# Optimization experiments

Hardware: AMD Instinct MI355X
Metric: run time of the kernel (lower is better)

Reference implementation:

```python
import jax, jax.numpy as jnp
import numpy as np

D_MODEL = 1024
N_HEAD = 16
D_HEAD = D_MODEL // N_HEAD
D_FF = 4096
B, S = 2, 2048
EPS = 1e-5


def setup_inputs() -> dict:
    key = jax.random.key(0)
    ks = jax.random.split(key, 16)
    sc = 1.0 / np.sqrt(D_MODEL)
    x = jax.random.normal(ks[0], (B, S, D_MODEL), dtype=jnp.float32)
    # causal mask: 1 where attention is disallowed (upper triangle)
    mask = jnp.triu(jnp.ones((S, S), dtype=jnp.int32), k=1)[None, None]
    p = {
        'x': x,
        'mask': mask,
        'wq': jax.random.normal(ks[1], (D_MODEL, D_MODEL), jnp.float32) * sc,
        'bq': jnp.zeros((D_MODEL,), jnp.float32),
        'wk': jax.random.normal(ks[2], (D_MODEL, D_MODEL), jnp.float32) * sc,
        'bk': jnp.zeros((D_MODEL,), jnp.float32),
        'wv': jax.random.normal(ks[3], (D_MODEL, D_MODEL), jnp.float32) * sc,
        'bv': jnp.zeros((D_MODEL,), jnp.float32),
        'wo': jax.random.normal(ks[4], (D_MODEL, D_MODEL), jnp.float32) * sc,
        'bo': jnp.zeros((D_MODEL,), jnp.float32),
        'w1': jax.random.normal(ks[5], (D_MODEL, D_FF), jnp.float32) * sc,
        'b1': jnp.zeros((D_FF,), jnp.float32),
        'w2': jax.random.normal(ks[6], (D_FF, D_MODEL), jnp.float32) * (1.0 / np.sqrt(D_FF)),
        'b2': jnp.zeros((D_MODEL,), jnp.float32),
        'g1': jnp.ones((D_MODEL,), jnp.float32),
        'beta1': jnp.zeros((D_MODEL,), jnp.float32),
        'g2': jnp.ones((D_MODEL,), jnp.float32),
        'beta2': jnp.zeros((D_MODEL,), jnp.float32),
    }
    return p


def _layer_norm(x, g, b):
    mu = jnp.mean(x, axis=-1, keepdims=True)
    var = jnp.mean(jnp.square(x - mu), axis=-1, keepdims=True)
    return (x - mu) * jax.lax.rsqrt(var + EPS) * g + b


def reference(x, mask, wq, bq, wk, bk, wv, bv, wo, bo, w1, b1, w2, b2, g1, beta1, g2, beta2):
    b, s, _ = x.shape
    # QKV projections -> [B, H, S, Dh]
    q = (x @ wq + bq).reshape(b, s, N_HEAD, D_HEAD).transpose(0, 2, 1, 3)
    k = (x @ wk + bk).reshape(b, s, N_HEAD, D_HEAD).transpose(0, 2, 1, 3)
    v = (x @ wv + bv).reshape(b, s, N_HEAD, D_HEAD).transpose(0, 2, 1, 3)
    scores = jnp.einsum('bhqd,bhkd->bhqk', q, k) / np.sqrt(D_HEAD)  # [B,H,S,S]
    scores = jnp.where(mask == 1, -jnp.inf, scores)
    attn = jax.nn.softmax(scores, axis=-1)
    out = jnp.einsum('bhqk,bhkd->bhqd', attn, v)
    out = out.transpose(0, 2, 1, 3).reshape(b, s, D_MODEL)
    attn_out = out @ wo + bo
    x1 = _layer_norm(x + attn_out, g1, beta1)
    ffn = jax.nn.relu(x1 @ w1 + b1) @ w2 + b2
    return _layer_norm(x1 + ffn, g2, beta2)
```

## Files before the change

### kernel.cpp

```cpp
#include <hip/hip_runtime.h>
#include <hip/hip_bf16.h>
#include <cstdint>

#define D_MODEL 1024
#define D_FF    4096
#define NHEAD   16
#define DHEAD   64
#define BATCH   2
#define SEQ     2048
#define BT      (BATCH*SEQ)
#define QKVLD   (3*D_MODEL)
#define LN_EPS  1e-5f

typedef __bf16 bf16_t;
typedef bf16_t bf16x8 __attribute__((ext_vector_type(8)));
typedef float  f32x4  __attribute__((ext_vector_type(4)));

__device__ __forceinline__ unsigned short f2b(float f){
  bf16_t h = (bf16_t)f;
  return __builtin_bit_cast(unsigned short, h);
}

__device__ __forceinline__ void gload16(const void* g, void* l){
  __builtin_amdgcn_global_load_lds(
      (const __attribute__((address_space(1))) unsigned int*)g,
      (__attribute__((address_space(3))) unsigned int*)l, 16, 0, 0);
}

__global__ __launch_bounds__(256) void cvt_f32_bf16(
    const float* __restrict__ in, unsigned short* __restrict__ out, int n){
  int i = (blockIdx.x*256 + threadIdx.x)*4;
  if (i < n){
    float4 v = *(const float4*)(in + i);
    ushort4 u; u.x=f2b(v.x); u.y=f2b(v.y); u.z=f2b(v.z); u.w=f2b(v.w);
    *(ushort4*)(out + i) = u;
  }
}

__global__ __launch_bounds__(256) void concat_bias(
    const float* __restrict__ bq, const float* __restrict__ bk,
    const float* __restrict__ bv, float* __restrict__ o){
  int i = blockIdx.x*256 + threadIdx.x;
  if (i < D_MODEL){ o[i]=bq[i]; o[D_MODEL+i]=bk[i]; o[2*D_MODEL+i]=bv[i]; }
}

__global__ __launch_bounds__(256) void transpose_cvt(
    const float* __restrict__ in, unsigned short* __restrict__ out, int R, int C){
  __shared__ float t[32][33];
  int c0 = blockIdx.x*32, r0 = blockIdx.y*32;
  int tx = threadIdx.x, ty = threadIdx.y;
  #pragma unroll
  for (int i=0;i<4;++i){ int r = ty + i*8; t[r][tx] = in[(size_t)(r0+r)*C + c0+tx]; }
  __syncthreads();
  #pragma unroll
  for (int i=0;i<4;++i){ int r = ty + i*8; out[(size_t)(c0+r)*R + r0+tx] = f2b(t[tx][r]); }
}

__global__ __launch_bounds__(256) void transpose_v(
    const unsigned short* __restrict__ QKV, unsigned short* __restrict__ Vt){
  __shared__ unsigned short t[32][33];
  int s0 = blockIdx.x*32, d0 = blockIdx.y*32, bh = blockIdx.z;
  int b = bh>>4, h = bh&15;
  int tx = threadIdx.x, ty = threadIdx.y;
  #pragma unroll
  for (int i=0;i<4;++i){ int r = ty + i*8;
    t[r][tx] = QKV[(size_t)(b*SEQ + s0+r)*QKVLD + 2*D_MODEL + h*DHEAD + d0+tx]; }
  __syncthreads();
  #pragma unroll
  for (int i=0;i<4;++i){ int r = ty + i*8;
    Vt[((size_t)bh*DHEAD + d0+r)*SEQ + s0+tx] = t[tx][r]; }
}

template<int EPI>
__global__ __launch_bounds__(512,4) void gemm128(
    const unsigned short* __restrict__ A, const unsigned short* __restrict__ Bt,
    const float* __restrict__ bias, const float* __restrict__ resid,
    float* __restrict__ outF, unsigned short* __restrict__ outB,
    int M, int N, int K){
  __shared__ __attribute__((aligned(16))) unsigned short As[2][128*64];
  __shared__ __attribute__((aligned(16))) unsigned short Bs[2][128*64];
  int tid = threadIdx.x;
  int lane = tid & 63, wave = tid >> 6;
  int lr = lane & 15, lg = lane >> 4;
  int row0 = blockIdx.x*128, col0 = blockIdx.y*128;
  int wr = (wave>>2)*64, wc = (wave&3)*32;
  int x7 = lr & 7;

  int sr = tid >> 3;
  int sl = (tid & 7) ^ (sr & 7);
  auto STAGE = [&](int k0, int buf){
    #pragma unroll
    for (int it=0; it<2; ++it){
      int c = it*512 + tid;
      int r = it*64 + sr;
      gload16(A  + (size_t)(row0+r)*K + k0 + sl*8, &As[buf][c<<3]);
      gload16(Bt + (size_t)(col0+r)*K + k0 + sl*8, &Bs[buf][c<<3]);
    }
  };

  f32x4 acc[4][2] = {};
  int nk = K >> 6;
  int t0 = 0, t1 = nk;
  if (EPI==3){ int half = nk >> 1; t0 = blockIdx.z*half; t1 = t0 + half; }
  STAGE(t0<<6, 0);
  asm volatile("s_waitcnt vmcnt(0)" ::: "memory");
  __builtin_amdgcn_s_barrier();
  int cur = 0;
  for (int t=t0; t<t1; ++t){
    if (t+1 < t1) STAGE((t+1)<<6, cur^1);
    #pragma unroll
    for (int kk=0; kk<2; ++kk){
      int sk = ((kk*4 + lg) ^ x7) << 3;
      bf16x8 af[4], bfr[2];
      #pragma unroll
      for (int mi=0;mi<4;++mi) af[mi]  = *(const bf16x8*)&As[cur][(wr+mi*16+lr)*64 + sk];
      #pragma unroll
      for (int ni=0;ni<2;++ni) bfr[ni] = *(const bf16x8*)&Bs[cur][(wc+ni*16+lr)*64 + sk];
      #pragma unroll
      for (int mi=0;mi<4;++mi)
        #pragma unroll
        for (int ni=0;ni<2;++ni)
          acc[mi][ni] = __builtin_amdgcn_mfma_f32_16x16x32_bf16(af[mi], bfr[ni], acc[mi][ni], 0,0,0);
    }
    asm volatile("s_waitcnt vmcnt(0)" ::: "memory");
    __builtin_amdgcn_s_barrier();
    cur ^= 1;
  }
  float* outP = (EPI==3) ? (outF + (size_t)blockIdx.z*((size_t)M*N)) : outF;
  #pragma unroll
  for (int mi=0;mi<4;++mi){
    int row = row0 + wr + mi*16 + (lg<<2);
    #pragma unroll
    for (int ni=0;ni<2;++ni){
      int col = col0 + wc + ni*16 + lr;
      float bs = (EPI==3) ? 0.f : bias[col];
      #pragma unroll
      for (int j=0;j<4;++j){
        size_t idx = (size_t)(row+j)*N + col;
        float v = acc[mi][ni][j] + bs;
        if (EPI==3){ outP[idx] = v; }
        else if (EPI==2){ v = fmaxf(v, 0.f); outB[idx] = f2b(v); }
        else { outB[idx] = f2b(v); }
      }
    }
  }
}

__global__ __launch_bounds__(256,2) void attn_k(
    const unsigned short* __restrict__ QKV,
    const unsigned short* __restrict__ Vt, unsigned short* __restrict__ O){
  __shared__ __attribute__((aligned(16))) unsigned short Ks[2][128*64];
  __shared__ __attribute__((aligned(16))) unsigned short Vs[2][64*128];
  __shared__ __attribute__((aligned(16))) unsigned short Ps[4][16*128];
  int tid = threadIdx.x, lane = tid&63, wave = tid>>6;
  int lr = lane&15, lg = lane>>4;
  int bid = blockIdx.x;
  int L = (bid & 7)*64 + (bid >> 3);
  int qx = L & 15;
  int bh = L >> 4;
  int b = bh>>4, h = bh&15;
  const int NT = SEQ/64;
  const float SC2 = 0.18033688011112042f;

  #pragma unroll 1
  for (int half=0; half<2; ++half){
    int qt = half ? qx : (NT-1 - qx);
    int q0w = qt*64 + wave*16;

    const unsigned short* Qrow = QKV + (size_t)(b*SEQ + q0w + lr)*QKVLD + h*DHEAD;
    bf16x8 qf[2];
    qf[0] = *(const bf16x8*)(Qrow + lg*8);
    qf[1] = *(const bf16x8*)(Qrow + 32 + lg*8);

    f32x4 oacc[4] = {};
    float m2 = -1e30f, lsum = 0.f;

    auto STAGE = [&](int t, int buf){
      int kv0 = t*128;
      #pragma unroll
      for (int it=0; it<4; ++it){
        int c = it*256 + tid;
        int rk = c>>3, slk = (c&7) ^ (rk&7);
        gload16(QKV + (size_t)(b*SEQ + kv0 + rk)*QKVLD + D_MODEL + h*DHEAD + slk*8, &Ks[buf][c<<3]);
        int rv = c>>4, slv = (c&15) ^ (rv&15);
        gload16(Vt + ((size_t)bh*DHEAD + rv)*SEQ + kv0 + slv*8, &Vs[buf][c<<3]);
      }
    };

    int nkv = (qt + 2) >> 1;
    STAGE(0, 0);
    asm volatile("s_waitcnt vmcnt(0)" ::: "memory");
    __builtin_amdgcn_s_barrier();
    int cur = 0;
    for (int t=0; t<nkv; ++t){
      if (t+1 < nkv) STAGE(t+1, cur^1);

      int kv0 = t*128;
      f32x4 sacc[8] = {};
      #pragma unroll
      for (int kk=0;kk<2;++kk){
        #pragma unroll
        for (int ni=0;ni<8;++ni){
          int krow = ni*16 + lr;
          bf16x8 kf = *(const bf16x8*)&Ks[cur][krow*64 + (((kk*4+lg) ^ (krow&7))<<3)];
          sacc[ni] = __builtin_amdgcn_mfma_f32_16x16x32_bf16(kf, qf[kk], sacc[ni], 0,0,0);
        }
      }
      if (t == nkv-1){
        int qpos = q0w + lr;
        #pragma unroll
        for (int ni=0;ni<8;++ni){
          f32x4 v = sacc[ni];
          #pragma unroll
          for (int j=0;j<4;++j){
            int kpos = kv0 + ni*16 + lg*4 + j;
            float sv = v[j]*SC2;
            v[j] = (kpos > qpos) ? -1e30f : sv;
          }
          sacc[ni] = v;
        }
      } else {
        #pragma unroll
        for (int ni=0;ni<8;++ni) sacc[ni] *= SC2;
      }
      f32x4 vm = sacc[0];
      #pragma unroll
      for (int ni=1;ni<8;++ni)
        #pragma unroll
        for (int j=0;j<4;++j) vm[j] = fmaxf(vm[j], sacc[ni][j]);
      float rm = fmaxf(fmaxf(vm[0],vm[1]), fmaxf(vm[2],vm[3]));
      rm = fmaxf(rm, __shfl_xor(rm, 16));
      rm = fmaxf(rm, __shfl_xor(rm, 32));
      float mnew = fmaxf(m2, rm);
      float corr = exp2f(m2 - mnew);
      m2 = mnew;
      f32x4 vs = {};
      #pragma unroll
      for (int ni=0;ni<8;++ni){
        f32x4 p;
        #pragma unroll
        for (int j=0;j<4;++j){ p[j] = exp2f(sacc[ni][j] - mnew); vs[j] += p[j]; }
        sacc[ni] = p;
      }
      float rs = (vs[0]+vs[1]) + (vs[2]+vs[3]);
      rs += __shfl_xor(rs, 16);
      rs += __shfl_xor(rs, 32);
      lsum = lsum*corr + rs;
      #pragma unroll
      for (int j=0;j<4;++j){
        float cj = __shfl(corr, lg*4 + j);
        #pragma unroll
        for (int nd=0; nd<4; ++nd) oacc[nd][j] *= cj;
      }
      #pragma unroll
      for (int ni=0;ni<8;++ni){
        ushort4 u; u.x=f2b(sacc[ni][0]); u.y=f2b(sacc[ni][1]);
                   u.z=f2b(sacc[ni][2]); u.w=f2b(sacc[ni][3]);
        int ts = ni*2 + (lg>>1);
        int a = lr*128 + (((ts ^ lr))<<3) + ((lg&1)<<2);
        *(uint2*)&Ps[wave][a] = __builtin_bit_cast(uint2, u);
      }
      #pragma unroll
      for (int kk=0;kk<4;++kk){
        bf16x8 pa = *(const bf16x8*)&Ps[wave][lr*128 + (((kk*4+lg) ^ lr)<<3)];
        #pragma unroll
        for (int nd=0; nd<4; ++nd){
          int dr = nd*16 + lr;
          bf16x8 vf = *(const bf16x8*)&Vs[cur][dr*128 + (((kk*4+lg) ^ (dr&15))<<3)];
          oacc[nd] = __builtin_amdgcn_mfma_f32_16x16x32_bf16(pa, vf, oacc[nd], 0,0,0);
        }
      }
      asm volatile("s_waitcnt vmcnt(0)" ::: "memory");
      __builtin_amdgcn_s_barrier();
      cur ^= 1;
    }
    #pragma unroll
    for (int j=0;j<4;++j){
      float lj = __shfl(lsum, lg*4 + j);
      float inv = 1.f / lj;
      int token = b*SEQ + q0w + lg*4 + j;
      #pragma unroll
      for (int nd=0; nd<4; ++nd)
        O[(size_t)token*D_MODEL + h*DHEAD + nd*16 + lr] = f2b(oacc[nd][j]*inv);
    }
  }
}

template<int MODE>
__global__ __launch_bounds__(256) void ln_sum_k(
    const float* __restrict__ P,
    const float* __restrict__ bias,
    const float* __restrict__ resid,
    const float* __restrict__ g, const float* __restrict__ bta,
    float* __restrict__ outF, unsigned short* __restrict__ outB){
  int row = blockIdx.x, tid = threadIdx.x;
  const size_t MN = (size_t)BT*D_MODEL;
  float4 p0 = ((const float4*)(P + (size_t)row*D_MODEL))[tid];
  float4 p1 = ((const float4*)(P + MN + (size_t)row*D_MODEL))[tid];
  float4 rr = ((const float4*)(resid + (size_t)row*D_MODEL))[tid];
  float4 bb = ((const float4*)bias)[tid];
  float4 v;
  v.x = p0.x+p1.x+bb.x+rr.x; v.y = p0.y+p1.y+bb.y+rr.y;
  v.z = p0.z+p1.z+bb.z+rr.z; v.w = p0.w+p1.w+bb.w+rr.w;
  float s = v.x+v.y+v.z+v.w;
  float q = v.x*v.x+v.y*v.y+v.z*v.z+v.w*v.w;
  #pragma unroll
  for (int d=32; d; d>>=1){ s += __shfl_xor(s, d); q += __shfl_xor(q, d); }
  __shared__ float rs[4], rq[4];
  int wave = tid>>6;
  if ((tid&63)==0){ rs[wave]=s; rq[wave]=q; }
  __syncthreads();
  s = rs[0]+rs[1]+rs[2]+rs[3];
  q = rq[0]+rq[1]+rq[2]+rq[3];
  float mu  = s * (1.f/D_MODEL);
  float var = q * (1.f/D_MODEL) - mu*mu;
  float rstd = rsqrtf(var + LN_EPS);
  float4 gg = ((const float4*)g)[tid];
  float4 be = ((const float4*)bta)[tid];
  float o0 = (v.x-mu)*rstd*gg.x + be.x;
  float o1 = (v.y-mu)*rstd*gg.y + be.y;
  float o2 = (v.z-mu)*rstd*gg.z + be.z;
  float o3 = (v.w-mu)*rstd*gg.w + be.w;
  float4 o; o.x=o0; o.y=o1; o.z=o2; o.w=o3;
  ((float4*)(outF + (size_t)row*D_MODEL))[tid] = o;
  if (MODE==0){
    ushort4 u; u.x=f2b(o0); u.y=f2b(o1); u.z=f2b(o2); u.w=f2b(o3);
    ((ushort4*)(outB + (size_t)row*D_MODEL))[tid] = u;
  }
}

extern "C" void kernel_launch(void* const* d_in, const int* in_sizes, int n_in,
                              void* d_out, int out_size, void* d_ws, size_t ws_size,
                              hipStream_t stream){
  const float* x  = (const float*)d_in[0];
  const float* wq = (const float*)d_in[2];  const float* bq = (const float*)d_in[3];
  const float* wk = (const float*)d_in[4];  const float* bk = (const float*)d_in[5];
  const float* wv = (const float*)d_in[6];  const float* bv = (const float*)d_in[7];
  const float* wo = (const float*)d_in[8];  const float* bo = (const float*)d_in[9];
  const float* w1 = (const float*)d_in[10]; const float* b1 = (const float*)d_in[11];
  const float* w2 = (const float*)d_in[12]; const float* b2 = (const float*)d_in[13];
  const float* g1 = (const float*)d_in[14]; const float* be1= (const float*)d_in[15];
  const float* g2 = (const float*)d_in[16]; const float* be2= (const float*)d_in[17];

  char* w = (char*)d_ws;
  size_t off = 0;
  auto nxt = [&](size_t bytes)->void*{
    void* p = w + off; off = (off + bytes + 255) & ~(size_t)255; return p;
  };
  unsigned short* xb    = (unsigned short*)nxt((size_t)BT*D_MODEL*2);
  unsigned short* wqkvT = (unsigned short*)nxt((size_t)QKVLD*D_MODEL*2);
  unsigned short* woT   = (unsigned short*)nxt((size_t)D_MODEL*D_MODEL*2);
  unsigned short* w1T   = (unsigned short*)nxt((size_t)D_MODEL*D_FF*2);
  unsigned short* w2T   = (unsigned short*)nxt((size_t)D_MODEL*D_FF*2);
  float*          bqkv  = (float*)nxt((size_t)QKVLD*4);
  unsigned short* QKV   = (unsigned short*)nxt((size_t)BT*QKVLD*2);
  unsigned short* VtG   = (unsigned short*)nxt((size_t)BT*D_MODEL*2);
  unsigned short* attnb = (unsigned short*)nxt((size_t)BT*D_MODEL*2);
  float*          x1f   = (float*)nxt((size_t)BT*D_MODEL*4);
  unsigned short* ffn1  = (unsigned short*)nxt((size_t)BT*D_FF*2);
  float*          Psum  = (float*)QKV;
  unsigned short* x1b   = attnb;

  dim3 tb(32,8);
  cvt_f32_bf16<<<(BT*D_MODEL)/1024, 256, 0, stream>>>(x, xb, BT*D_MODEL);
  concat_bias<<<4, 256, 0, stream>>>(bq, bk, bv, bqkv);
  transpose_cvt<<<dim3(D_MODEL/32, D_MODEL/32), tb, 0, stream>>>(wq, wqkvT,                    D_MODEL, D_MODEL);
  transpose_cvt<<<dim3(D_MODEL/32, D_MODEL/32), tb, 0, stream>>>(wk, wqkvT + D_MODEL*D_MODEL,  D_MODEL, D_MODEL);
  transpose_cvt<<<dim3(D_MODEL/32, D_MODEL/32), tb, 0, stream>>>(wv, wqkvT + 2*D_MODEL*D_MODEL,D_MODEL, D_MODEL);
  transpose_cvt<<<dim3(D_MODEL/32, D_MODEL/32), tb, 0, stream>>>(wo, woT, D_MODEL, D_MODEL);
  transpose_cvt<<<dim3(D_FF/32,    D_MODEL/32), tb, 0, stream>>>(w1, w1T, D_MODEL, D_FF);
  transpose_cvt<<<dim3(D_MODEL/32, D_FF/32),    tb, 0, stream>>>(w2, w2T, D_FF, D_MODEL);

  gemm128<0><<<dim3(BT/128, QKVLD/128), 512, 0, stream>>>(xb, wqkvT, bqkv, nullptr, nullptr, QKV, BT, QKVLD, D_MODEL);

  transpose_v<<<dim3(SEQ/32, DHEAD/32, BATCH*NHEAD), tb, 0, stream>>>(QKV, VtG);
  attn_k<<<512, 256, 0, stream>>>(QKV, VtG, attnb);

  gemm128<3><<<dim3(BT/128, D_MODEL/128, 2), 512, 0, stream>>>(attnb, woT, nullptr, nullptr, Psum, nullptr, BT, D_MODEL, D_MODEL);
  ln_sum_k<0><<<BT, 256, 0, stream>>>(Psum, bo, x, g1, be1, x1f, x1b);

  gemm128<2><<<dim3(BT/128, D_FF/128), 512, 0, stream>>>(x1b, w1T, b1, nullptr, nullptr, ffn1, BT, D_FF, D_MODEL);

  gemm128<3><<<dim3(BT/128, D_MODEL/128, 2), 512, 0, stream>>>(ffn1, w2T, nullptr, nullptr, Psum, nullptr, BT, D_MODEL, D_FF);
  ln_sum_k<1><<<BT, 256, 0, stream>>>(Psum, b2, x1f, g2, be2, (float*)d_out, nullptr);
}
```

Baseline: 233.5 us.

## Give each attention wave two query groups and single-buffer V

The attention kernel now processes one 128-row query tile per block, with 32 rows per wave, instead of two 64-row tiles in a paired causal half loop. Each K/V fragment read from LDS feeds two MFMAs, which halves LDS traffic per unit of compute. V is single-buffered and its next tile is loaded after the PV stage, and the waits are relaxed to vmcnt(4) so K prefetch overlaps compute. The trade-offs are causal load imbalance across blocks (tile lengths range 1..16), higher register pressure, and V loads no longer overlapping the PV stage.

```diff
diff --git a/kernel.cpp b/kernel.cpp
--- a/kernel.cpp
+++ b/kernel.cpp
@@ -150,140 +150,163 @@
     const unsigned short* __restrict__ QKV,
     const unsigned short* __restrict__ Vt, unsigned short* __restrict__ O){
   __shared__ __attribute__((aligned(16))) unsigned short Ks[2][128*64];
-  __shared__ __attribute__((aligned(16))) unsigned short Vs[2][64*128];
-  __shared__ __attribute__((aligned(16))) unsigned short Ps[4][16*128];
+  __shared__ __attribute__((aligned(16))) unsigned short Vs[64*128];
+  __shared__ __attribute__((aligned(16))) unsigned short Ps[4][2][16*128];
   int tid = threadIdx.x, lane = tid&63, wave = tid>>6;
   int lr = lane&15, lg = lane>>4;
   int bid = blockIdx.x;
   int L = (bid & 7)*64 + (bid >> 3);
-  int qx = L & 15;
   int bh = L >> 4;
+  int qrank = L & 15;
+  int qt = 15 - qrank;
   int b = bh>>4, h = bh&15;
-  const int NT = SEQ/64;
+  int q0 = qt*128 + wave*32;
   const float SC2 = 0.18033688011112042f;
 
-  #pragma unroll 1
-  for (int half=0; half<2; ++half){
-    int qt = half ? qx : (NT-1 - qx);
-    int q0w = qt*64 + wave*16;
-
-    const unsigned short* Qrow = QKV + (size_t)(b*SEQ + q0w + lr)*QKVLD + h*DHEAD;
-    bf16x8 qf[2];
-    qf[0] = *(const bf16x8*)(Qrow + lg*8);
-    qf[1] = *(const bf16x8*)(Qrow + 32 + lg*8);
-
-    f32x4 oacc[4] = {};
-    float m2 = -1e30f, lsum = 0.f;
-
-    auto STAGE = [&](int t, int buf){
-      int kv0 = t*128;
-      #pragma unroll
-      for (int it=0; it<4; ++it){
-        int c = it*256 + tid;
-        int rk = c>>3, slk = (c&7) ^ (rk&7);
-        gload16(QKV + (size_t)(b*SEQ + kv0 + rk)*QKVLD + D_MODEL + h*DHEAD + slk*8, &Ks[buf][c<<3]);
-        int rv = c>>4, slv = (c&15) ^ (rv&15);
-        gload16(Vt + ((size_t)bh*DHEAD + rv)*SEQ + kv0 + slv*8, &Vs[buf][c<<3]);
-      }
-    };
-
-    int nkv = (qt + 2) >> 1;
-    STAGE(0, 0);
-    asm volatile("s_waitcnt vmcnt(0)" ::: "memory");
-    __builtin_amdgcn_s_barrier();
-    int cur = 0;
-    for (int t=0; t<nkv; ++t){
-      if (t+1 < nkv) STAGE(t+1, cur^1);
-
-      int kv0 = t*128;
-      f32x4 sacc[8] = {};
-      #pragma unroll
-      for (int kk=0;kk<2;++kk){
+  bf16x8 qf[2][2];
+  #pragma unroll
+  for (int g=0; g<2; ++g)
+    #pragma unroll
+    for (int kk=0; kk<2; ++kk)
+      qf[g][kk] = *(const bf16x8*)&QKV[(size_t)(b*SEQ + q0 + g*16 + lr)*QKVLD + h*DHEAD + kk*32 + lg*8];
+
+  f32x4 oacc[2][4] = {};
+  float m2[2] = {-1e30f, -1e30f}, lsum[2] = {0.f, 0.f};
+
+  auto STAGE_K = [&](int t, int buf){
+    int kv0 = t*128;
+    #pragma unroll
+    for (int it=0; it<4; ++it){
+      int c = it*256 + tid;
+      int rk = c>>3, slk = (c&7) ^ (rk&7);
+      gload16(QKV + (size_t)(b*SEQ + kv0 + rk)*QKVLD + D_MODEL + h*DHEAD + slk*8, &Ks[buf][c<<3]);
+    }
+  };
+  auto STAGE_V = [&](int t){
+    int kv0 = t*128;
+    #pragma unroll
+    for (int it=0; it<4; ++it){
+      int c = it*256 + tid;
+      int rv = c>>4, slv = (c&15) ^ (rv&15);
+      gload16(Vt + ((size_t)bh*DHEAD + rv)*SEQ + kv0 + slv*8, &Vs[c<<3]);
+    }
+  };
+
+  int nkv = qt + 1;
+  STAGE_K(0, 0);
+  STAGE_V(0);
+  asm volatile("s_waitcnt vmcnt(0)" ::: "memory");
+  __builtin_amdgcn_s_barrier();
+  int cur = 0;
+  for (int t=0; t<nkv; ++t){
+    bool pre = (t+1 < nkv);
+    if (pre) STAGE_K(t+1, cur^1);
+
+    int kv0 = t*128;
+    f32x4 sacc[2][8] = {};
+    #pragma unroll
+    for (int kk=0;kk<2;++kk){
+      #pragma unroll
+      for (int ni=0;ni<8;++ni){
+        int krow = ni*16 + lr;
+        bf16x8 kf = *(const bf16x8*)&Ks[cur][krow*64 + (((kk*4+lg) ^ (krow&7))<<3)];
+        sacc[0][ni] = __builtin_amdgcn_mfma_f32_16x16x32_bf16(kf, qf[0][kk], sacc[0][ni], 0,0,0);
+        sacc[1][ni] = __builtin_amdgcn_mfma_f32_16x16x32_bf16(kf, qf[1][kk], sacc[1][ni], 0,0,0);
+      }
+    }
+    if (t == nkv-1){
+      #pragma unroll
+      for (int g=0;g<2;++g){
+        int qpos = q0 + g*16 + lr;
         #pragma unroll
         for (int ni=0;ni<8;++ni){
-          int krow = ni*16 + lr;
-          bf16x8 kf = *(const bf16x8*)&Ks[cur][krow*64 + (((kk*4+lg) ^ (krow&7))<<3)];
-          sacc[ni] = __builtin_amdgcn_mfma_f32_16x16x32_bf16(kf, qf[kk], sacc[ni], 0,0,0);
-        }
-      }
-      if (t == nkv-1){
-        int qpos = q0w + lr;
-        #pragma unroll
-        for (int ni=0;ni<8;++ni){
-          f32x4 v = sacc[ni];
+          f32x4 v = sacc[g][ni];
           #pragma unroll
           for (int j=0;j<4;++j){
             int kpos = kv0 + ni*16 + lg*4 + j;
             float sv = v[j]*SC2;
             v[j] = (kpos > qpos) ? -1e30f : sv;
           }
-          sacc[ni] = v;
+          sacc[g][ni] = v;
         }
-      } else {
-        #pragma unroll
-        for (int ni=0;ni<8;++ni) sacc[ni] *= SC2;
-      }
-      f32x4 vm = sacc[0];
+      }
+    } else {
+      #pragma unroll
+      for (int g=0;g<2;++g)
+        #pragma unroll
+        for (int ni=0;ni<8;++ni) sacc[g][ni] *= SC2;
+    }
+    #pragma unroll
+    for (int g=0;g<2;++g){
+      f32x4 vm = sacc[g][0];
       #pragma unroll
       for (int ni=1;ni<8;++ni)
         #pragma unroll
-        for (int j=0;j<4;++j) vm[j] = fmaxf(vm[j], sacc[ni][j]);
+        for (int j=0;j<4;++j) vm[j] = fmaxf(vm[j], sacc[g][ni][j]);
       float rm = fmaxf(fmaxf(vm[0],vm[1]), fmaxf(vm[2],vm[3]));
       rm = fmaxf(rm, __shfl_xor(rm, 16));
       rm = fmaxf(rm, __shfl_xor(rm, 32));
-      float mnew = fmaxf(m2, rm);
-      float corr = exp2f(m2 - mnew);
-      m2 = mnew;
+      float mnew = fmaxf(m2[g], rm);
+      float corr = exp2f(m2[g] - mnew);
+      m2[g] = mnew;
       f32x4 vs = {};
       #pragma unroll
       for (int ni=0;ni<8;++ni){
         f32x4 p;
         #pragma unroll
-        for (int j=0;j<4;++j){ p[j] = exp2f(sacc[ni][j] - mnew); vs[j] += p[j]; }
-        sacc[ni] = p;
+        for (int j=0;j<4;++j){ p[j] = exp2f(sacc[g][ni][j] - mnew); vs[j] += p[j]; }
+        sacc[g][ni] = p;
       }
       float rs = (vs[0]+vs[1]) + (vs[2]+vs[3]);
       rs += __shfl_xor(rs, 16);
       rs += __shfl_xor(rs, 32);
-      lsum = lsum*corr + rs;
+      lsum[g] = lsum[g]*corr + rs;
       #pragma unroll
       for (int j=0;j<4;++j){
         float cj = __shfl(corr, lg*4 + j);
         #pragma unroll
-        for (int nd=0; nd<4; ++nd) oacc[nd][j] *= cj;
+        for (int nd=0; nd<4; ++nd) oacc[g][nd][j] *= cj;
       }
       #pragma unroll
       for (int ni=0;ni<8;++ni){
-        ushort4 u; u.x=f2b(sacc[ni][0]); u.y=f2b(sacc[ni][1]);
-                   u.z=f2b(sacc[ni][2]); u.w=f2b(sacc[ni][3]);
+        ushort4 u; u.x=f2b(sacc[g][ni][0]); u.y=f2b(sacc[g][ni][1]);
+                   u.z=f2b(sacc[g][ni][2]); u.w=f2b(sacc[g][ni][3]);
         int ts = ni*2 + (lg>>1);
-        int a = lr*128 + (((ts ^ lr))<<3) + ((lg&1)<<2);
-        *(uint2*)&Ps[wave][a] = __builtin_bit_cast(uint2, u);
-      }
-      #pragma unroll
-      for (int kk=0;kk<4;++kk){
-        bf16x8 pa = *(const bf16x8*)&Ps[wave][lr*128 + (((kk*4+lg) ^ lr)<<3)];
-        #pragma unroll
-        for (int nd=0; nd<4; ++nd){
-          int dr = nd*16 + lr;
-          bf16x8 vf = *(const bf16x8*)&Vs[cur][dr*128 + (((kk*4+lg) ^ (dr&15))<<3)];
-          oacc[nd] = __builtin_amdgcn_mfma_f32_16x16x32_bf16(pa, vf, oacc[nd], 0,0,0);
-        }
-      }
-      asm volatile("s_waitcnt vmcnt(0)" ::: "memory");
-      __builtin_amdgcn_s_barrier();
-      cur ^= 1;
-    }
+        int a = lr*128 + ((ts ^ lr)<<3) + ((lg&1)<<2);
+        *(uint2*)&Ps[wave][g][a] = __builtin_bit_cast(uint2, u);
+      }
+    }
+    if (pre){ asm volatile("s_waitcnt vmcnt(4)" ::: "memory"); }
+    else    { asm volatile("s_waitcnt vmcnt(0)" ::: "memory"); }
+    __builtin_amdgcn_s_barrier();
+    #pragma unroll
+    for (int kk=0;kk<4;++kk){
+      bf16x8 paA = *(const bf16x8*)&Ps[wave][0][lr*128 + (((kk*4+lg) ^ lr)<<3)];
+      bf16x8 paB = *(const bf16x8*)&Ps[wave][1][lr*128 + (((kk*4+lg) ^ lr)<<3)];
+      #pragma unroll
+      for (int nd=0; nd<4; ++nd){
+        int dr = nd*16 + lr;
+        bf16x8 vf = *(const bf16x8*)&Vs[dr*128 + (((kk*4+lg) ^ (dr&15))<<3)];
+        oacc[0][nd] = __builtin_amdgcn_mfma_f32_16x16x32_bf16(paA, vf, oacc[0][nd], 0,0,0);
+        oacc[1][nd] = __builtin_amdgcn_mfma_f32_16x16x32_bf16(paB, vf, oacc[1][nd], 0,0,0);
+      }
+    }
+    asm volatile("s_waitcnt vmcnt(0)" ::: "memory");
+    __builtin_amdgcn_s_barrier();
+    if (pre) STAGE_V(t+1);
+    cur ^= 1;
+  }
+  #pragma unroll
+  for (int g=0;g<2;++g)
     #pragma unroll
     for (int j=0;j<4;++j){
-      float lj = __shfl(lsum, lg*4 + j);
+      float lj = __shfl(lsum[g], lg*4 + j);
       float inv = 1.f / lj;
-      int token = b*SEQ + q0w + lg*4 + j;
+      int token = b*SEQ + q0 + g*16 + lg*4 + j;
       #pragma unroll
       for (int nd=0; nd<4; ++nd)
-        O[(size_t)token*D_MODEL + h*DHEAD + nd*16 + lr] = f2b(oacc[nd][j]*inv);
-    }
-  }
+        O[(size_t)token*D_MODEL + h*DHEAD + nd*16 + lr] = f2b(oacc[g][nd][j]*inv);
+    }
 }
 
 template<int MODE>
```

Measured after the change: 258.8 us. 10.8% more time.

## Add 256x256-tile GEMM with staged prefetch for QKV and FFN1 projections

Applied to the files above, without the earlier changes.

Adds a new GEMM kernel with 256x256 output tiles per 512-thread block. Each wave computes a 128x64 sub-tile in four quarter phases, and next-k-tile loads are interleaved between MFMA phases under s_setprio. The QKV and FFN-up GEMMs use it instead of the 128x128 kernel, which raises arithmetic intensity and cuts global/LDS traffic per FLOP. In exchange it uses 128KB of LDS per block and more accumulator registers, and launches fewer blocks (192 for QKV, 256 for FFN1), which may underfill the GPU's compute units.

```diff
diff --git a/kernel.cpp b/kernel.cpp
--- a/kernel.cpp
+++ b/kernel.cpp
@@ -141,6 +141,141 @@
         if (EPI==3){ outP[idx] = v; }
         else if (EPI==2){ v = fmaxf(v, 0.f); outB[idx] = f2b(v); }
         else { outB[idx] = f2b(v); }
+      }
+    }
+  }
+}
+
+template<int EPI>
+__global__ __launch_bounds__(512,2) void gemm256(
+    const unsigned short* __restrict__ A, const unsigned short* __restrict__ Bt,
+    const float* __restrict__ bias, unsigned short* __restrict__ outB,
+    int M, int N, int K){
+  __shared__ __attribute__((aligned(16))) unsigned short As[2][2][128*64];
+  __shared__ __attribute__((aligned(16))) unsigned short Bs[2][2][128*64];
+  int tid = threadIdx.x;
+  int lane = tid & 63, wave = tid >> 6;
+  int lr = lane & 15, lg = lane >> 4;
+  int wm = wave >> 2, wn = wave & 3;
+  int row0 = blockIdx.x*256, col0 = blockIdx.y*256;
+  int x7 = lr & 7;
+  int sr = tid >> 3;
+  int sl = (tid & 7) ^ (sr & 7);
+
+  auto STAGE_A = [&](int t, int buf, int h){
+    #pragma unroll
+    for (int i=0;i<2;++i){
+      int c = i*512 + tid;
+      int r = i*64 + sr;
+      gload16(A + (size_t)(row0 + h*128 + r)*K + t*64 + sl*8, &As[buf][h][c<<3]);
+    }
+  };
+  auto STAGE_B = [&](int t, int buf, int h){
+    #pragma unroll
+    for (int i=0;i<2;++i){
+      int c = i*512 + tid;
+      int r = i*64 + sr;
+      gload16(Bt + (size_t)(col0 + h*128 + r)*K + t*64 + sl*8, &Bs[buf][h][c<<3]);
+    }
+  };
+
+  f32x4 acc[8][4] = {};
+  int nk = K >> 6;
+  STAGE_B(0,0,0); STAGE_B(0,0,1); STAGE_A(0,0,0); STAGE_A(0,0,1);
+  asm volatile("s_waitcnt vmcnt(0)" ::: "memory");
+  __builtin_amdgcn_s_barrier();
+  int cur = 0;
+  int bq = (wn&1)*64;
+  for (int t=0; t<nk; ++t){
+    bool pre = (t+1 < nk);
+    const unsigned short* Ah = &As[cur][wm][0];
+    const unsigned short* Bh = &Bs[cur][wn>>1][0];
+    bf16x8 af[4][2], bfr[4][2];
+    #pragma unroll
+    for (int mi=0;mi<4;++mi)
+      #pragma unroll
+      for (int kk=0;kk<2;++kk)
+        af[mi][kk] = *(const bf16x8*)&Ah[(mi*16+lr)*64 + (((kk*4+lg)^x7)<<3)];
+    #pragma unroll
+    for (int ni=0;ni<2;++ni)
+      #pragma unroll
+      for (int kk=0;kk<2;++kk)
+        bfr[ni][kk] = *(const bf16x8*)&Bh[(bq+ni*16+lr)*64 + (((kk*4+lg)^x7)<<3)];
+    if (pre){ STAGE_B(t+1, cur^1, 0);
+              asm volatile("s_waitcnt vmcnt(2)" ::: "memory"); }
+    else    { asm volatile("s_waitcnt vmcnt(0)" ::: "memory"); }
+    __builtin_amdgcn_s_barrier();
+    __builtin_amdgcn_s_setprio(1);
+    #pragma unroll
+    for (int mi=0;mi<4;++mi)
+      #pragma unroll
+      for (int ni=0;ni<2;++ni)
+        #pragma unroll
+        for (int kk=0;kk<2;++kk)
+          acc[mi][ni] = __builtin_amdgcn_mfma_f32_16x16x32_bf16(af[mi][kk], bfr[ni][kk], acc[mi][ni], 0,0,0);
+    __builtin_amdgcn_s_setprio(0);
+    __builtin_amdgcn_s_barrier();
+    #pragma unroll
+    for (int ni=2;ni<4;++ni)
+      #pragma unroll
+      for (int kk=0;kk<2;++kk)
+        bfr[ni][kk] = *(const bf16x8*)&Bh[(bq+ni*16+lr)*64 + (((kk*4+lg)^x7)<<3)];
+    if (pre) STAGE_B(t+1, cur^1, 1);
+    __builtin_amdgcn_s_barrier();
+    __builtin_amdgcn_s_setprio(1);
+    #pragma unroll
+    for (int mi=0;mi<4;++mi)
+      #pragma unroll
+      for (int ni=2;ni<4;++ni)
+        #pragma unroll
+        for (int kk=0;kk<2;++kk)
+          acc[mi][ni] = __builtin_amdgcn_mfma_f32_16x16x32_bf16(af[mi][kk], bfr[ni][kk], acc[mi][ni], 0,0,0);
+    __builtin_amdgcn_s_setprio(0);
+    __builtin_amdgcn_s_barrier();
+    #pragma unroll
+    for (int mi=0;mi<4;++mi)
+      #pragma unroll
+      for (int kk=0;kk<2;++kk)
+        af[mi][kk] = *(const bf16x8*)&Ah[((mi+4)*16+lr)*64 + (((kk*4+lg)^x7)<<3)];
+    if (pre) STAGE_A(t+1, cur^1, 0);
+    __builtin_amdgcn_s_barrier();
+    __builtin_amdgcn_s_setprio(1);
+    #pragma unroll
+    for (int mi=0;mi<4;++mi)
+      #pragma unroll
+      for (int ni=0;ni<2;++ni)
+        #pragma unroll
+        for (int kk=0;kk<2;++kk)
+          acc[mi+4][ni] = __builtin_amdgcn_mfma_f32_16x16x32_bf16(af[mi][kk], bfr[ni][kk], acc[mi+4][ni], 0,0,0);
+    __builtin_amdgcn_s_setprio(0);
+    __builtin_amdgcn_s_barrier();
+    if (pre) STAGE_A(t+1, cur^1, 1);
+    __builtin_amdgcn_s_barrier();
+    __builtin_amdgcn_s_setprio(1);
+    #pragma unroll
+    for (int mi=0;mi<4;++mi)
+      #pragma unroll
+      for (int ni=2;ni<4;++ni)
+        #pragma unroll
+        for (int kk=0;kk<2;++kk)
+          acc[mi+4][ni] = __builtin_amdgcn_mfma_f32_16x16x32_bf16(af[mi][kk], bfr[ni][kk], acc[mi+4][ni], 0,0,0);
+    __builtin_amdgcn_s_setprio(0);
+    __builtin_amdgcn_s_barrier();
+    cur ^= 1;
+  }
+  #pragma unroll
+  for (int mi=0;mi<8;++mi){
+    int row = row0 + wm*128 + mi*16 + (lg<<2);
+    #pragma unroll
+    for (int ni=0;ni<4;++ni){
+      int col = col0 + wn*64 + ni*16 + lr;
+      float bs = bias[col];
+      #pragma unroll
+      for (int j=0;j<4;++j){
+        size_t idx = (size_t)(row+j)*N + col;
+        float v = acc[mi][ni][j] + bs;
+        if (EPI==2) v = fmaxf(v, 0.f);
+        outB[idx] = f2b(v);
       }
     }
   }
@@ -371,7 +506,7 @@
   transpose_cvt<<<dim3(D_FF/32,    D_MODEL/32), tb, 0, stream>>>(w1, w1T, D_MODEL, D_FF);
   transpose_cvt<<<dim3(D_MODEL/32, D_FF/32),    tb, 0, stream>>>(w2, w2T, D_FF, D_MODEL);
 
-  gemm128<0><<<dim3(BT/128, QKVLD/128), 512, 0, stream>>>(xb, wqkvT, bqkv, nullptr, nullptr, QKV, BT, QKVLD, D_MODEL);
+  gemm256<0><<<dim3(BT/256, QKVLD/256), 512, 0, stream>>>(xb, wqkvT, bqkv, QKV, BT, QKVLD, D_MODEL);
 
   transpose_v<<<dim3(SEQ/32, DHEAD/32, BATCH*NHEAD), tb, 0, stream>>>(QKV, VtG);
   attn_k<<<512, 256, 0, stream>>>(QKV, VtG, attnb);
@@ -379,7 +514,7 @@
   gemm128<3><<<dim3(BT/128, D_MODEL/128, 2), 512, 0, stream>>>(attnb, woT, nullptr, nullptr, Psum, nullptr, BT, D_MODEL, D_MODEL);
   ln_sum_k<0><<<BT, 256, 0, stream>>>(Psum, bo, x, g1, be1, x1f, x1b);
 
-  gemm128<2><<<dim3(BT/128, D_FF/128), 512, 0, stream>>>(x1b, w1T, b1, nullptr, nullptr, ffn1, BT, D_FF, D_MODEL);
+  gemm256<2><<<dim3(BT/256, D_FF/256), 512, 0, stream>>>(x1b, w1T, b1, ffn1, BT, D_FF, D_MODEL);
 
   gemm128<3><<<dim3(BT/128, D_MODEL/128, 2), 512, 0, stream>>>(ffn1, w2T, nullptr, nullptr, Psum, nullptr, BT, D_MODEL, D_FF);
   ln_sum_k<1><<<BT, 256, 0, stream>>>(Psum, b2, x1f, g2, be2, (float*)d_out, nullptr);
```

Result: no change. 229.4 us (-1.8%).
